# Kernel optimization log

Hardware: AMD Instinct MI355X
Metric: run time of the kernel (lower is better)

Reference implementation:

```python
import jax, jax.numpy as jnp
import numpy as np

C = 768
E = 32
H = 4 * C

def setup_inputs() -> dict:
    key = jax.random.key(0)
    ks = jax.random.split(key, 5)
    B, T = 2, 1024
    scale_in = 1.0 / np.sqrt(C)
    scale_hid = 1.0 / np.sqrt(H)
    return {
        "x": jax.random.normal(ks[0], (B, T, C), jnp.float32),
        "gate_w": jax.random.normal(ks[1], (C, E), jnp.float32) * scale_in,
        "gate_b": jnp.zeros((E,), jnp.float32),
        "w1": jax.random.normal(ks[2], (E, C, H), jnp.float32) * scale_in,
        "b1": jnp.zeros((E, H), jnp.float32),
        "w2": jax.random.normal(ks[3], (E, H, C), jnp.float32) * scale_hid,
        "b2": jnp.zeros((E, C), jnp.float32),
    }

def reference(x, gate_w, gate_b, w1, b1, w2, b2):
    # gates: [B, T, E] softmax over experts
    gates = jax.nn.softmax(x @ gate_w + gate_b, axis=-1)
    # all-expert FFN: h [B, T, E, H]
    h = jax.nn.gelu(jnp.einsum('btc,ech->bteh', x, w1) + b1, approximate=False)
    # expert outputs [B, T, E, C]
    y = jnp.einsum('bteh,ehc->btec', h, w2) + b2
    # gate-weighted sum over experts -> [B, T, C]  (dropout = identity in eval)
    out = jnp.einsum('bte,btec->btc', gates, y)
    return out
```

## Files before the change

kernel.cpp:

```cpp
#include <hip/hip_runtime.h>
#include <stdint.h>


typedef unsigned short u16;
typedef __attribute__((ext_vector_type(8))) short short8;
typedef __attribute__((ext_vector_type(8))) unsigned short ushort8v;
typedef __attribute__((ext_vector_type(4))) unsigned short ushort4v;
typedef __attribute__((ext_vector_type(4))) float float4v;

#define DEV __device__ __forceinline__

DEV u16 rne_bf16(float f) {
  union { float f; uint32_t u; } v; v.f = f;
  uint32_t u = v.u;
  u += 0x7FFFu + ((u >> 16) & 1u);
  return (u16)(u >> 16);
}

DEV float fast_erf(float x) {
  float ax = __builtin_fabsf(x);
  float t = __builtin_amdgcn_rcpf(__builtin_fmaf(0.3275911f, ax, 1.0f));
  float p = t * (0.254829592f + t * (-0.284496736f + t * (1.421413741f +
            t * (-1.453152027f + t * 1.061405429f))));
  float r = 1.0f - p * __expf(-ax * ax);
  return __builtin_copysignf(r, x);
}

DEV void load_lds16(const void* g, void* l) {
  __builtin_amdgcn_global_load_lds(
      (const __attribute__((address_space(1))) unsigned int*)g,
      (__attribute__((address_space(3))) unsigned int*)l,
      16, 0, 0);
}


__global__ void cvt_x_kernel(const float* __restrict__ x, u16* __restrict__ xb, int n4) {
  int i = blockIdx.x * 256 + threadIdx.x;
  if (i >= n4) return;
  float4v v = *(const float4v*)(x + (size_t)i * 4);
  ushort4v o;
  o[0] = rne_bf16(v[0]); o[1] = rne_bf16(v[1]);
  o[2] = rne_bf16(v[2]); o[3] = rne_bf16(v[3]);
  *(ushort4v*)(xb + (size_t)i * 4) = o;
}

__global__ void gate_kernel(const float* __restrict__ x, const float* __restrict__ gw,
                            const float* __restrict__ gb, float* __restrict__ gates) {
  int lane = threadIdx.x;
  int tok = blockIdx.x * 2 + (lane >> 5);
  int e = lane & 31;
  const float* xr = x + (size_t)tok * 768;
  float s = gb[e];
  #pragma unroll 4
  for (int c = 0; c < 768; ++c) s += xr[c] * gw[c * 32 + e];
  float mx = s;
  #pragma unroll
  for (int o = 16; o >= 1; o >>= 1) mx = fmaxf(mx, __shfl_xor(mx, o, 32));
  float ex = __expf(s - mx);
  float sum = ex;
  #pragma unroll
  for (int o = 16; o >= 1; o >>= 1) sum += __shfl_xor(sum, o, 32);
  gates[tok * 32 + e] = ex / sum;
}

__global__ void bias_out_kernel(const float* __restrict__ gates, const float* __restrict__ b2,
                                float* __restrict__ out) {
  int idx = blockIdx.x * 256 + threadIdx.x;
  int n = idx / 768;
  int c = idx - n * 768;
  const float* g = gates + n * 32;
  float s = 0.f;
  #pragma unroll
  for (int e = 0; e < 32; ++e) s += g[e] * b2[e * 768 + c];
  out[idx] = s;
}

__global__ void reduce_kernel(const float* __restrict__ part, const float* __restrict__ gates,
                              float* __restrict__ out, int zn, int e_base, int n4) {
  int i = blockIdx.x * 256 + threadIdx.x;
  if (i >= n4) return;
  int n = (i << 2) / 768;
  const float* g = gates + n * 32 + e_base;
  float4v o = *(const float4v*)(out + (size_t)i * 4);
  #pragma unroll 4
  for (int z = 0; z < zn; ++z) {
    float gz = g[z];
    float4v p = *(const float4v*)(part + (size_t)z * (2048L * 768) + (size_t)i * 4);
    o[0] += gz * p[0]; o[1] += gz * p[1]; o[2] += gz * p[2]; o[3] += gz * p[3];
  }
  *(float4v*)(out + (size_t)i * 4) = o;
}

__global__ void pack_b_kernel(const float* __restrict__ in, u16* __restrict__ out,
                              int ktiles, int n_per_e, long e_stride, int row_stride) {
  int kt = blockIdx.x, nt = blockIdx.y;
  int n0 = nt * 128;
  int e = n0 / n_per_e;
  int nl = n0 - e * n_per_e;
  const float* src = in + (long)e * e_stride + (long)kt * 64 * row_stride + nl;

  __shared__ u16 lds[64 * 136];
  int t = threadIdx.x;
  {
    int k = t >> 2, nq = (t & 3) * 32;
    const float* p = src + (long)k * row_stride + nq;
    u16 tmp[32];
    #pragma unroll
    for (int i = 0; i < 32; i += 4) {
      float4v v = *(const float4v*)(p + i);
      tmp[i] = rne_bf16(v[0]); tmp[i + 1] = rne_bf16(v[1]);
      tmp[i + 2] = rne_bf16(v[2]); tmp[i + 3] = rne_bf16(v[3]);
    }
    #pragma unroll
    for (int i = 0; i < 32; i += 8)
      *(ushort8v*)&lds[k * 136 + nq + i] = *(ushort8v*)&tmp[i];
  }
  __syncthreads();
  {
    int n = t >> 1, half = t & 1;
    u16 v[32];
    #pragma unroll
    for (int j = 0; j < 32; ++j) v[j] = lds[(half * 32 + j) * 136 + n];
    u16* tile = out + ((long)nt * ktiles + kt) * 8192 + n * 64;
    int sw = n & 7;
    #pragma unroll
    for (int cc = 0; cc < 4; ++cc) {
      int c = half * 4 + cc;
      *(ushort8v*)(tile + ((c ^ sw) * 8)) = *(ushort8v*)&v[cc * 8];
    }
  }
}

template <int MODE>
__global__ __launch_bounds__(512, 2) void gemm256(
    const u16* __restrict__ A, long lda,
    const u16* __restrict__ Bp, int ktt, int ktb, int nkt,
    void* __restrict__ outp, long ldo,
    const float* __restrict__ b1g, long zstride) {

  extern __shared__ u16 sm[];
  u16* const Abuf[2] = { sm,         sm + 32768 };
  u16* const Bbuf[2] = { sm + 16384, sm + 49152 };

  const int tid  = threadIdx.x;
  const int wave = tid >> 6, lane = tid & 63;
  const int wr = wave >> 2, wc = wave & 3;
  const int bh = wave >> 2, w4 = wave & 3;
  const int lr = lane >> 3, l8 = lane & 7;
  const int frow = lane & 15, fq = lane >> 4, fx = lane & 7;
  const int m0 = blockIdx.x * 256;
  const int nt0 = blockIdx.y * 2;
  const int kt_begin = blockIdx.z * ktb;

  const u16* gA = A + (long)(m0 + wave * 32 + lr) * lda + (long)kt_begin * 64 + (l8 ^ lr) * 8;
  const u16* gB = Bp + ((long)(nt0 + bh) * ktt + kt_begin) * 8192 + w4 * 2048 + lane * 8;
  u16* const ldsA[2] = { Abuf[0] + wave * 2048, Abuf[1] + wave * 2048 };
  u16* const ldsB[2] = { Bbuf[0] + bh * 8192 + w4 * 2048, Bbuf[1] + bh * 8192 + w4 * 2048 };

  float4v acc[8][4] = {};
  short8 af[4][2], bf[2][2];

#define STAGE(p) { \
    _Pragma("unroll") for (int j = 0; j < 4; ++j) { \
      load_lds16(gA + (long)j * 8 * lda, ldsA[p] + j * 512); \
      load_lds16(gB + j * 512,           ldsB[p] + j * 512); } \
    gA += 64; gB += 8192; }

#define RD_A(p, QM) \
    _Pragma("unroll") for (int mf = 0; mf < 4; ++mf) \
    _Pragma("unroll") for (int ks = 0; ks < 2; ++ks) \
      af[mf][ks] = *(const short8*)&Abuf[p][(wr * 128 + (QM) * 64 + mf * 16 + frow) * 64 + \
                                            (((ks * 4 + fq) ^ fx) * 8)];

#define RD_B(p, QN) \
    _Pragma("unroll") for (int nf = 0; nf < 2; ++nf) \
    _Pragma("unroll") for (int ks = 0; ks < 2; ++ks) \
      bf[nf][ks] = *(const short8*)&Bbuf[p][(wc * 64 + (QN) * 32 + nf * 16 + frow) * 64 + \
                                            (((ks * 4 + fq) ^ fx) * 8)];

#define MMQ(QM, QN) { \
    __builtin_amdgcn_s_barrier(); \
    asm volatile("s_waitcnt lgkmcnt(0)" ::: "memory"); \
    __builtin_amdgcn_sched_barrier(0); \
    __builtin_amdgcn_s_setprio(1); \
    _Pragma("unroll") for (int mf = 0; mf < 4; ++mf) \
    _Pragma("unroll") for (int nf = 0; nf < 2; ++nf) \
    _Pragma("unroll") for (int ks = 0; ks < 2; ++ks) \
      acc[(QM) * 4 + mf][(QN) * 2 + nf] = __builtin_amdgcn_mfma_f32_16x16x32_bf16( \
          af[mf][ks], bf[nf][ks], acc[(QM) * 4 + mf][(QN) * 2 + nf], 0, 0, 0); \
    __builtin_amdgcn_s_setprio(0); \
    __builtin_amdgcn_s_barrier(); }

#define HALF(p) { RD_A(p, 0); RD_B(p, 0); MMQ(0, 0); \
                  RD_B(p, 1);             MMQ(0, 1); \
                  RD_A(p, 1);             MMQ(1, 1); \
                  RD_B(p, 0);             MMQ(1, 0); }

#define WAITV8 { asm volatile("s_waitcnt vmcnt(8)" ::: "memory"); \
                 __builtin_amdgcn_s_barrier(); __builtin_amdgcn_sched_barrier(0); }
#define WAITV0 { asm volatile("s_waitcnt vmcnt(0)" ::: "memory"); \
                 __builtin_amdgcn_s_barrier(); __builtin_amdgcn_sched_barrier(0); }

  STAGE(0); STAGE(1);
  const int niter = nkt >> 1;
  for (int i = 0; i < niter - 1; ++i) {
    WAITV8;
    HALF(0);
    STAGE(0);
    WAITV8;
    HALF(1);
    STAGE(1);
  }
  WAITV8; HALF(0);
  WAITV0; HALF(1);

#undef STAGE
#undef RD_A
#undef RD_B
#undef MMQ
#undef HALF
#undef WAITV8
#undef WAITV0

  if (MODE == 1) {
    const int n0 = nt0 * 128;
    const int e_loc = n0 / 3072;
    const int h0 = n0 - e_loc * 3072;
    const float* be = b1g + (long)e_loc * 3072 + h0;
    u16* out = (u16*)outp;
    #pragma unroll
    for (int qn = 0; qn < 2; ++qn)
      #pragma unroll
      for (int nf = 0; nf < 2; ++nf) {
        const int ncol = wc * 64 + qn * 32 + nf * 16 + frow;
        const float bv = be[ncol];
        #pragma unroll
        for (int qm = 0; qm < 2; ++qm)
          #pragma unroll
          for (int mf = 0; mf < 4; ++mf) {
            u16* op = out + (long)(m0 + wr * 128 + qm * 64 + mf * 16 + fq * 4) * ldo + (n0 + ncol);
            #pragma unroll
            for (int r = 0; r < 4; ++r) {
              float v = acc[qm * 4 + mf][qn * 2 + nf][r] + bv;
              v = 0.5f * v * (1.0f + fast_erf(v * 0.70710678118654752440f));
              op[(long)r * ldo] = rne_bf16(v);
            }
          }
      }
  } else {
    float* out = (float*)outp + (long)blockIdx.z * zstride;
    const int n0 = nt0 * 128;
    #pragma unroll
    for (int qn = 0; qn < 2; ++qn)
      #pragma unroll
      for (int nf = 0; nf < 2; ++nf) {
        const int ncol = n0 + wc * 64 + qn * 32 + nf * 16 + frow;
        #pragma unroll
        for (int qm = 0; qm < 2; ++qm)
          #pragma unroll
          for (int mf = 0; mf < 4; ++mf) {
            float* op = out + (long)(m0 + wr * 128 + qm * 64 + mf * 16 + fq * 4) * ldo + ncol;
            #pragma unroll
            for (int r = 0; r < 4; ++r) op[(long)r * ldo] = acc[qm * 4 + mf][qn * 2 + nf][r];
          }
      }
  }
}


extern "C" void kernel_launch(void* const* d_in, const int* in_sizes, int n_in,
                              void* d_out, int out_size, void* d_ws, size_t ws_size,
                              hipStream_t stream) {
  (void)in_sizes; (void)n_in; (void)out_size;
  const float* x  = (const float*)d_in[0];
  const float* gw = (const float*)d_in[1];
  const float* gb = (const float*)d_in[2];
  const float* w1 = (const float*)d_in[3];
  const float* b1 = (const float*)d_in[4];
  const float* w2 = (const float*)d_in[5];
  const float* b2 = (const float*)d_in[6];
  float* out = (float*)d_out;

  const long N = 2048, C = 768, H = 3072;

  int G = 32;
  for (;;) {
    long need = N * C * 2 + N * 32 * 4 + (long)G * N * C * 4
              + (long)G * C * H * 2 * 2 + N * (long)G * H * 2;
    if ((size_t)need <= ws_size || G == 1) break;
    G >>= 1;
  }

  char* p = (char*)d_ws;
  u16*   xb    = (u16*)p;   p += N * C * 2;
  float* gates = (float*)p; p += N * 32 * 4;
  float* parts = (float*)p; p += (long)G * N * C * 4;
  u16*   w1b   = (u16*)p;   p += (long)G * C * H * 2;
  u16*   w2b   = (u16*)p;   p += (long)G * H * C * 2;
  u16*   hbuf  = (u16*)p;

  hipFuncSetAttribute(reinterpret_cast<const void*>(gemm256<1>),
                      hipFuncAttributeMaxDynamicSharedMemorySize, 131072);
  hipFuncSetAttribute(reinterpret_cast<const void*>(gemm256<2>),
                      hipFuncAttributeMaxDynamicSharedMemorySize, 131072);

  cvt_x_kernel<<<(N * C / 4 + 255) / 256, 256, 0, stream>>>(x, xb, (int)(N * C / 4));
  gate_kernel<<<N / 2, 64, 0, stream>>>(x, gw, gb, gates);
  bias_out_kernel<<<N * C / 256, 256, 0, stream>>>(gates, b2, out);

  const int ngroups = 32 / G;
  for (int g = 0; g < ngroups; ++g) {
    const float* w1g = w1 + (long)g * G * C * H;
    const float* w2g = w2 + (long)g * G * H * C;

    dim3 pg1(12, 24 * G);
    pack_b_kernel<<<pg1, 256, 0, stream>>>(w1g, w1b, 12, (int)H, (long)C * H, (int)H);

    gemm256<1><<<dim3(8, 12 * G, 1), 512, 131072, stream>>>(
        xb, C, w1b, 12, 0, 12, (void*)hbuf, (long)G * H, b1 + (long)g * G * H, 0L);

    dim3 pg2(48 * G, 6);
    pack_b_kernel<<<pg2, 256, 0, stream>>>(w2g, w2b, 48 * G, 768, 0L, 768);

    gemm256<2><<<dim3(8, 3, G), 512, 131072, stream>>>(
        hbuf, (long)G * H, w2b, 48 * G, 48, 48, (void*)parts, 768L, nullptr, N * C);

    reduce_kernel<<<(int)((N * C / 4 + 255) / 256), 256, 0, stream>>>(
        parts, gates, out, G, g * G, (int)(N * C / 4));
  }
}
```

Baseline: 1.669 ms.

## Swizzle block IDs across XCDs and coalesce GELU epilogue stores via LDS

```diff
diff --git a/kernel.cpp b/kernel.cpp
--- a/kernel.cpp
+++ b/kernel.cpp
@@ -148,9 +148,19 @@
   const int bh = wave >> 2, w4 = wave & 3;
   const int lr = lane >> 3, l8 = lane & 7;
   const int frow = lane & 15, fq = lane >> 4, fx = lane & 7;
-  const int m0 = blockIdx.x * 256;
-  const int nt0 = blockIdx.y * 2;
-  const int kt_begin = blockIdx.z * ktb;
+
+  const int gx = gridDim.x, gy = gridDim.y;
+  int id = blockIdx.x + gx * (blockIdx.y + gy * blockIdx.z);
+  const int total = gx * gy * (int)gridDim.z;
+  id = (id & 7) * (total >> 3) + (id >> 3);
+  const int bxi = id % gx;
+  const int rest = id / gx;
+  const int byi = rest % gy;
+  const int bzi = rest / gy;
+
+  const int m0 = bxi * 256;
+  const int nt0 = byi * 2;
+  const int kt_begin = bzi * ktb;
 
   const u16* gA = A + (long)(m0 + wave * 32 + lr) * lda + (long)kt_begin * 64 + (l8 ^ lr) * 8;
   const u16* gB = Bp + ((long)(nt0 + bh) * ktt + kt_begin) * 8192 + w4 * 2048 + lane * 8;
@@ -226,29 +236,42 @@
     const int n0 = nt0 * 128;
     const int e_loc = n0 / 3072;
     const int h0 = n0 - e_loc * 3072;
-    const float* be = b1g + (long)e_loc * 3072 + h0;
+    const float* be = b1g + (long)e_loc * 3072 + h0 + wc * 64;
     u16* out = (u16*)outp;
+    u16* scr = sm + wave * 1024;
+    float bvv[2][2];
     #pragma unroll
     for (int qn = 0; qn < 2; ++qn)
       #pragma unroll
-      for (int nf = 0; nf < 2; ++nf) {
-        const int ncol = wc * 64 + qn * 32 + nf * 16 + frow;
-        const float bv = be[ncol];
+      for (int nf = 0; nf < 2; ++nf)
+        bvv[qn][nf] = be[qn * 32 + nf * 16 + frow];
+
+    #pragma unroll
+    for (int qm = 0; qm < 2; ++qm)
+      #pragma unroll
+      for (int mf = 0; mf < 4; ++mf) {
         #pragma unroll
-        for (int qm = 0; qm < 2; ++qm)
+        for (int qn = 0; qn < 2; ++qn)
           #pragma unroll
-          for (int mf = 0; mf < 4; ++mf) {
-            u16* op = out + (long)(m0 + wr * 128 + qm * 64 + mf * 16 + fq * 4) * ldo + (n0 + ncol);
+          for (int nf = 0; nf < 2; ++nf) {
+            const int c = qn * 32 + nf * 16 + frow;
             #pragma unroll
             for (int r = 0; r < 4; ++r) {
-              float v = acc[qm * 4 + mf][qn * 2 + nf][r] + bv;
+              float v = acc[qm * 4 + mf][qn * 2 + nf][r] + bvv[qn][nf];
               v = 0.5f * v * (1.0f + fast_erf(v * 0.70710678118654752440f));
-              op[(long)r * ldo] = rne_bf16(v);
+              scr[(fq * 4 + r) * 64 + c] = rne_bf16(v);
             }
           }
+        #pragma unroll
+        for (int h = 0; h < 2; ++h) {
+          const int row = h * 8 + (lane >> 3);
+          ushort8v vv = *(const ushort8v*)&scr[row * 64 + (lane & 7) * 8];
+          *(ushort8v*)(out + (long)(m0 + wr * 128 + qm * 64 + mf * 16 + row) * ldo
+                           + (n0 + wc * 64 + (lane & 7) * 8)) = vv;
+        }
       }
   } else {
-    float* out = (float*)outp + (long)blockIdx.z * zstride;
+    float* out = (float*)outp + (long)bzi * zstride;
     const int n0 = nt0 * 128;
     #pragma unroll
     for (int qn = 0; qn < 2; ++qn)
```

After: 1.545 ms. 7.4% less time.
